# Kernel optimization log

Hardware: AMD Instinct MI355X
Metric: run time of the kernel (lower is better)

The kernel has to match this reference:

```python
import jax, jax.numpy as jnp
import numpy as np

B, LQ, C = 2, 12240, 256
NH, NL, NP = 8, 4, 4          # heads, levels, points
D = C // NH                   # head dim = 32
SHAPES = np.array([[96, 96], [48, 48], [24, 24], [12, 12]], dtype=np.int32)
LEN_IN = int((SHAPES[:, 0] * SHAPES[:, 1]).sum())  # 12240


def setup_inputs() -> dict:
    key = jax.random.key(0)
    ks = jax.random.split(key, 10)
    start = np.concatenate([[0], np.cumsum(SHAPES[:, 0] * SHAPES[:, 1])[:-1]]).astype(np.int32)
    return {
        "query": jax.random.normal(ks[0], (B, LQ, C), jnp.float32),
        "reference_points": jax.random.uniform(ks[1], (B, LQ, NL, 2), jnp.float32),
        "input_flatten": jax.random.normal(ks[2], (B, LEN_IN, C), jnp.float32),
        "input_spatial_shapes": jnp.asarray(SHAPES),
        "input_level_start_index": jnp.asarray(start),
        # params (sampling_offsets weight kept small so samples land near the reference point)
        "W_off": jax.random.normal(ks[3], (C, NH * NL * NP * 2), jnp.float32) * 0.01,
        "b_off": jax.random.normal(ks[4], (NH * NL * NP * 2,), jnp.float32) * 0.1,
        "W_attn": jax.random.normal(ks[5], (C, NH * NL * NP), jnp.float32) * 0.02,
        "b_attn": jnp.zeros((NH * NL * NP,), jnp.float32),
        "W_val": jax.random.normal(ks[6], (C, C), jnp.float32) * (1.0 / np.sqrt(C)),
        "b_val": jnp.zeros((C,), jnp.float32),
        "W_out": jax.random.normal(ks[7], (C, C), jnp.float32) * (1.0 / np.sqrt(C)),
        "b_out": jnp.zeros((C,), jnp.float32),
    }


def _bilinear_sample(v, loc):
    """grid_sample(align_corners=False, padding=zeros) equivalent.
    v:   (B, Hl, Wl, NH, D) level feature map per head
    loc: (B, Lq, NH, NP, 2) normalized sampling locations in [0,1]
    ->   (B, Lq, NH, NP, D)
    """
    _, Hl, Wl, _, _ = v.shape
    x = loc[..., 0] * Wl - 0.5
    y = loc[..., 1] * Hl - 0.5
    x0 = jnp.floor(x); y0 = jnp.floor(y)
    lx = x - x0;       ly = y - y0
    x0i = x0.astype(jnp.int32); y0i = y0.astype(jnp.int32)
    bi = jnp.arange(v.shape[0])[:, None, None, None]
    hi = jnp.arange(NH)[None, None, :, None]

    def gather(yi, xi):
        valid = (yi >= 0) & (yi < Hl) & (xi >= 0) & (xi < Wl)
        yc = jnp.clip(yi, 0, Hl - 1)
        xc = jnp.clip(xi, 0, Wl - 1)
        g = v[bi, yc, xc, hi]                       # (B,Lq,NH,NP,D)
        return g * valid[..., None].astype(v.dtype)

    w00 = (1 - lx) * (1 - ly); w01 = lx * (1 - ly)
    w10 = (1 - lx) * ly;       w11 = lx * ly
    return (gather(y0i, x0i) * w00[..., None] + gather(y0i, x0i + 1) * w01[..., None]
            + gather(y0i + 1, x0i) * w10[..., None] + gather(y0i + 1, x0i + 1) * w11[..., None])


def reference(query, reference_points, input_flatten, input_spatial_shapes,
              input_level_start_index, W_off, b_off, W_attn, b_attn,
              W_val, b_val, W_out, b_out):
    shapes = np.asarray(input_spatial_shapes)          # static level geometry
    starts = np.asarray(input_level_start_index)

    value = (input_flatten @ W_val + b_val).reshape(B, LEN_IN, NH, D)
    offsets = (query @ W_off + b_off).reshape(B, LQ, NH, NL, NP, 2)
    attn = (query @ W_attn + b_attn).reshape(B, LQ, NH, NL * NP)
    attn = jax.nn.softmax(attn, axis=-1).reshape(B, LQ, NH, NL, NP)

    # normalizer is (W_l, H_l) per level
    normalizer = jnp.stack([input_spatial_shapes[:, 1], input_spatial_shapes[:, 0]], -1).astype(query.dtype)
    loc = (reference_points[:, :, None, :, None, :]
           + offsets / normalizer[None, None, None, :, None, :])  # (B,Lq,NH,NL,NP,2)

    out = jnp.zeros((B, LQ, NH, D), query.dtype)
    for l in range(NL):
        Hl, Wl = int(shapes[l, 0]), int(shapes[l, 1])
        s = int(starts[l])
        v_l = value[:, s:s + Hl * Wl].reshape(B, Hl, Wl, NH, D)
        sampled = _bilinear_sample(v_l, loc[:, :, :, l])            # (B,Lq,NH,NP,D)
        out = out + jnp.einsum("bqhpd,bqhp->bqhd", sampled, attn[:, :, :, l])
    out = out.reshape(B, LQ, C)
    return out @ W_out + b_out
```

## Files before the change

kernel.cpp:

```cpp
#include <hip/hip_runtime.h>
#include <math.h>

#define B_    2
#define LQ_   12240
#define C_    256
#define NH_   8
#define NL_   4
#define NP_   4
#define LEN_IN_ 12240
#define MROWS (B_*LQ_)
#define MF_   (MROWS/16)
#define KF_   8
#define APLANE ((size_t)MROWS * C_)
#define NBLK  383

typedef __attribute__((ext_vector_type(8))) short short8v;
typedef __attribute__((ext_vector_type(4))) float f32x4;
typedef __attribute__((ext_vector_type(2))) float f32x2;
typedef __attribute__((ext_vector_type(2))) uint  u32x2;

__device__ __forceinline__ ushort f2bf_hi(float f) {
    uint u = __builtin_bit_cast(uint, f);
    uint r = (u + 0x7fffu + ((u >> 16) & 1u)) >> 16;
    return (ushort)r;
}
__device__ __forceinline__ float bf2f(ushort h) {
    uint u = ((uint)h) << 16;
    return __builtin_bit_cast(float, u);
}

#define U4_VAL  0
#define U4_OFF  8192
#define U4_ATT  16384
#define U4_UHI  20480
#define U4_ULO  28672
#define PACKB_TOTAL 294912

__global__ __launch_bounds__(256) void pack_w_kernel(
    const float* __restrict__ Wv, const float* __restrict__ Wo,
    const float* __restrict__ Wa, const float* __restrict__ Wu,
    ushort* __restrict__ packB)
{
    int gid = blockIdx.x * 256 + threadIdx.x;
    if (gid >= 28672) return;
    const float* W; ushort* hi; ushort* lo = nullptr; int N, rel;
    if (gid < 8192)       { W = Wv; hi = packB;          N = 256; rel = gid; }
    else if (gid < 16384) { W = Wo; hi = packB + 65536;  N = 256; rel = gid - 8192; }
    else if (gid < 20480) { W = Wa; hi = packB + 131072; N = 128; rel = gid - 16384; }
    else { W = Wu; hi = packB + 163840; lo = packB + 229376; N = 256; rel = gid - 20480; }

    const int lane = rel & 63;
    const int kf   = (rel >> 6) & 7;
    const int nf   = rel >> 9;
    const int row0 = kf * 32 + (lane >> 4) * 8;
    const int col  = nf * 16 + (lane & 15);

    union { ushort u16[8]; uint4 u4; } ch, cl;
#pragma unroll
    for (int j = 0; j < 8; ++j) {
        float x = W[(size_t)(row0 + j) * N + col];
        ushort h = f2bf_hi(x);
        ch.u16[j] = h;
        cl.u16[j] = f2bf_hi(x - bf2f(h));
    }
    *reinterpret_cast<uint4*>(hi + (size_t)rel * 8) = ch.u4;
    if (lo) *reinterpret_cast<uint4*>(lo + (size_t)rel * 8) = cl.u4;
}

__global__ __launch_bounds__(512) void gemm_vq_kernel(
    const float* __restrict__ inflat, const float* __restrict__ query,
    const ushort* __restrict__ packB,
    const float* __restrict__ b_val, const float* __restrict__ b_off,
    const float* __restrict__ b_attn,
    ushort* __restrict__ valbf, float* __restrict__ offsb, float* __restrict__ attnb)
{
    const int t = threadIdx.x, lane = t & 63, wid = t >> 6;
    const int rowBase = blockIdx.x * 64;
    const bool isVal = (blockIdx.y == 0);
    const float* __restrict__ A = isVal ? inflat : query;

    __shared__ ushort Als[2048 * 8];

#pragma unroll
    for (int i = 0; i < 4; ++i) {
        int frag = i * 512 + t;
        int fl = frag & 63, kf = (frag >> 6) & 7, mf = frag >> 9;
        int row = min(rowBase + mf * 16 + (fl & 15), MROWS - 1);
        int k0 = kf * 32 + (fl >> 4) * 8;
        const float4* s = reinterpret_cast<const float4*>(A + (size_t)row * 256 + k0);
        float4 v0 = s[0], v1 = s[1];
        float vv[8] = { v0.x, v0.y, v0.z, v0.w, v1.x, v1.y, v1.z, v1.w };
        union { ushort u16[8]; uint4 u4; } hh;
#pragma unroll
        for (int j = 0; j < 8; ++j) hh.u16[j] = f2bf_hi(vv[j]);
        *reinterpret_cast<uint4*>(&Als[(size_t)frag * 8]) = hh.u4;
    }
    __syncthreads();

    const uint4* A4 = reinterpret_cast<const uint4*>(Als);
    const int colLane = lane & 15, rquad = lane >> 4;
    const int wnf = wid * 2;

    if (isVal) {
        const uint4* B4 = reinterpret_cast<const uint4*>(packB) + U4_VAL;
        f32x4 acc[4][2];
#pragma unroll
        for (int mi = 0; mi < 4; ++mi)
#pragma unroll
            for (int f = 0; f < 2; ++f) acc[mi][f] = (f32x4)0.0f;

#pragma unroll
        for (int kf = 0; kf < KF_; ++kf) {
            uint4 bh[2], ah[4];
#pragma unroll
            for (int f = 0; f < 2; ++f) bh[f] = B4[((wnf + f) * KF_ + kf) * 64 + lane];
#pragma unroll
            for (int mi = 0; mi < 4; ++mi) ah[mi] = A4[(mi * KF_ + kf) * 64 + lane];
#pragma unroll
            for (int mi = 0; mi < 4; ++mi) {
                short8v a = __builtin_bit_cast(short8v, ah[mi]);
#pragma unroll
                for (int f = 0; f < 2; ++f)
                    acc[mi][f] = __builtin_amdgcn_mfma_f32_16x16x32_bf16(
                        a, __builtin_bit_cast(short8v, bh[f]), acc[mi][f], 0, 0, 0);
            }
        }
#pragma unroll
        for (int f = 0; f < 2; ++f) {
            int col = (wnf + f) * 16 + colLane;
            float bv = b_val[col];
#pragma unroll
            for (int mi = 0; mi < 4; ++mi)
#pragma unroll
                for (int e = 0; e < 4; ++e) {
                    int row = rowBase + mi * 16 + rquad * 4 + e;
                    if (row < MROWS) valbf[(size_t)row * 256 + col] = f2bf_hi(acc[mi][f][e] + bv);
                }
        }
    } else {
        const uint4* BO = reinterpret_cast<const uint4*>(packB) + U4_OFF;
        const uint4* BA = reinterpret_cast<const uint4*>(packB) + U4_ATT;
        f32x4 acc[4][3];
#pragma unroll
        for (int mi = 0; mi < 4; ++mi)
#pragma unroll
            for (int f = 0; f < 3; ++f) acc[mi][f] = (f32x4)0.0f;

#pragma unroll
        for (int kf = 0; kf < KF_; ++kf) {
            uint4 bh[3], ah[4];
#pragma unroll
            for (int f = 0; f < 2; ++f) bh[f] = BO[((wnf + f) * KF_ + kf) * 64 + lane];
            bh[2] = BA[(wid * KF_ + kf) * 64 + lane];
#pragma unroll
            for (int mi = 0; mi < 4; ++mi) ah[mi] = A4[(mi * KF_ + kf) * 64 + lane];
#pragma unroll
            for (int mi = 0; mi < 4; ++mi) {
                short8v a = __builtin_bit_cast(short8v, ah[mi]);
#pragma unroll
                for (int f = 0; f < 3; ++f)
                    acc[mi][f] = __builtin_amdgcn_mfma_f32_16x16x32_bf16(
                        a, __builtin_bit_cast(short8v, bh[f]), acc[mi][f], 0, 0, 0);
            }
        }
#pragma unroll
        for (int f = 0; f < 2; ++f) {
            int col = (wnf + f) * 16 + colLane;
            float bv = b_off[col];
#pragma unroll
            for (int mi = 0; mi < 4; ++mi)
#pragma unroll
                for (int e = 0; e < 4; ++e) {
                    int row = rowBase + mi * 16 + rquad * 4 + e;
                    if (row < MROWS) offsb[(size_t)row * 256 + col] = acc[mi][f][e] + bv;
                }
        }
        {
            int col = wid * 16 + colLane;
            float bv = b_attn[col];
#pragma unroll
            for (int mi = 0; mi < 4; ++mi)
#pragma unroll
                for (int e = 0; e < 4; ++e) {
                    float v = acc[mi][2][e] + bv;
                    float mx = v;
#pragma unroll
                    for (int m = 8; m >= 1; m >>= 1) mx = fmaxf(mx, __shfl_xor(mx, m, 16));
                    float ex = __expf(v - mx);
                    float s = ex;
#pragma unroll
                    for (int m = 8; m >= 1; m >>= 1) s += __shfl_xor(s, m, 16);
                    int row = rowBase + mi * 16 + rquad * 4 + e;
                    if (row < MROWS) attnb[(size_t)row * 128 + col] = ex / s;
                }
        }
    }
}

__global__ __launch_bounds__(512) void gemm_out_kernel(
    const ushort* __restrict__ midH, const ushort* __restrict__ packB,
    const float* __restrict__ bias, float* __restrict__ Cg)
{
    const int t = threadIdx.x, lane = t & 63, wid = t >> 6;
    const int rowBase = blockIdx.x * 64;

    __shared__ ushort Ahs[2048 * 8];

    const uint4* H4 = reinterpret_cast<const uint4*>(midH);
#pragma unroll
    for (int i = 0; i < 4; ++i) {
        int frag = i * 512 + t;
        int fl = frag & 63, kf = (frag >> 6) & 7, mf = frag >> 9;
        int row = min(rowBase + mf * 16 + (fl & 15), MROWS - 1);
        int kq = kf * 4 + (fl >> 4);
        *reinterpret_cast<uint4*>(&Ahs[(size_t)frag * 8]) = H4[(size_t)row * 32 + kq];
    }
    __syncthreads();

    const uint4* BH4 = reinterpret_cast<const uint4*>(packB) + U4_UHI;
    const uint4* BL4 = reinterpret_cast<const uint4*>(packB) + U4_ULO;
    const uint4* A4 = reinterpret_cast<const uint4*>(Ahs);
    const int wnf = wid * 2;

    f32x4 acc[4][2];
#pragma unroll
    for (int mi = 0; mi < 4; ++mi)
#pragma unroll
        for (int f = 0; f < 2; ++f) acc[mi][f] = (f32x4)0.0f;

#pragma unroll
    for (int kf = 0; kf < KF_; ++kf) {
        uint4 bh[2], bl[2], ah[4];
#pragma unroll
        for (int f = 0; f < 2; ++f) {
            bh[f] = BH4[((wnf + f) * KF_ + kf) * 64 + lane];
            bl[f] = BL4[((wnf + f) * KF_ + kf) * 64 + lane];
        }
#pragma unroll
        for (int mi = 0; mi < 4; ++mi) ah[mi] = A4[(mi * KF_ + kf) * 64 + lane];
#pragma unroll
        for (int mi = 0; mi < 4; ++mi) {
            short8v a = __builtin_bit_cast(short8v, ah[mi]);
#pragma unroll
            for (int f = 0; f < 2; ++f) {
                acc[mi][f] = __builtin_amdgcn_mfma_f32_16x16x32_bf16(
                    a, __builtin_bit_cast(short8v, bh[f]), acc[mi][f], 0, 0, 0);
                acc[mi][f] = __builtin_amdgcn_mfma_f32_16x16x32_bf16(
                    a, __builtin_bit_cast(short8v, bl[f]), acc[mi][f], 0, 0, 0);
            }
        }
    }

    const int colLane = lane & 15, rquad = lane >> 4;
#pragma unroll
    for (int f = 0; f < 2; ++f) {
        int col = (wnf + f) * 16 + colLane;
        float bv = bias[col];
#pragma unroll
        for (int mi = 0; mi < 4; ++mi)
#pragma unroll
            for (int e = 0; e < 4; ++e) {
                int row = rowBase + mi * 16 + rquad * 4 + e;
                if (row < MROWS) Cg[(size_t)row * 256 + col] = acc[mi][f][e] + bv;
            }
    }
}

__global__ __launch_bounds__(128) void sampler_kernel(
    const ushort* __restrict__ value,
    const float* __restrict__ offs,
    const float* __restrict__ attnw,
    const float* __restrict__ refp,
    ushort* __restrict__ midH)
{
    const int t  = threadIdx.x;
    const int qi = t >> 6;
    const int t6 = t & 63;
    const int q  = blockIdx.x * 2 + qi;

    __shared__ float s_ref[2][8];
    __shared__ int   s_addr[2][576];
    __shared__ float s_w[2][576];

    if (t < 16) s_ref[t >> 3][t & 7] = refp[(size_t)(blockIdx.x * 2 + (t >> 3)) * 8 + (t & 7)];
    __syncthreads();

#pragma unroll
    for (int batch = 0; batch < 2; ++batch) {
        const int p  = t6 + batch * 64;
        const int h  = p >> 4;
        const int lp = p & 15;
        const int l  = lp >> 2;

        const float aw = attnw[(size_t)q * 128 + p];
        const float2 o = reinterpret_cast<const float2*>(offs)[(size_t)q * 128 + p];
        const float rx = s_ref[qi][l * 2 + 0];
        const float ry = s_ref[qi][l * 2 + 1];

        const int   Wl = 96 >> l;
        const int   st = 12288 - (12288 >> (2 * l));
        const float fW = (float)Wl;

        const float x = fmaf(rx, fW, o.x) - 0.5f;
        const float y = fmaf(ry, fW, o.y) - 0.5f;
        const float x0f = floorf(x), y0f = floorf(y);
        const float fx = x - x0f, fy = y - y0f;
        const int x0 = (int)x0f, y0 = (int)y0f;
        const int x1 = x0 + 1,   y1 = y0 + 1;

        const float vx0 = (x0 >= 0 && x0 < Wl) ? 1.f : 0.f;
        const float vx1 = (x1 >= 0 && x1 < Wl) ? 1.f : 0.f;
        const float vy0 = (y0 >= 0 && y0 < Wl) ? 1.f : 0.f;
        const float vy1 = (y1 >= 0 && y1 < Wl) ? 1.f : 0.f;

        const int xc0 = min(max(x0, 0), Wl - 1);
        const int xc1 = min(max(x1, 0), Wl - 1);
        const int yc0 = min(max(y0, 0), Wl - 1);
        const int yc1 = min(max(y1, 0), Wl - 1);

        const int row0 = st + yc0 * Wl;
        const int row1 = st + yc1 * Wl;
        const int hb   = h << 5;

        const int sidx = (lp * 9 + h) * 4;
        int4 a;
        a.x = ((row0 + xc0) << 8) + hb;
        a.y = ((row0 + xc1) << 8) + hb;
        a.z = ((row1 + xc0) << 8) + hb;
        a.w = ((row1 + xc1) << 8) + hb;
        *reinterpret_cast<int4*>(&s_addr[qi][sidx]) = a;

        float4 w;
        w.x = aw * (1.f - fx) * (1.f - fy) * vx0 * vy0;
        w.y = aw * fx * (1.f - fy) * vx1 * vy0;
        w.z = aw * (1.f - fx) * fy * vx0 * vy1;
        w.w = aw * fx * fy * vx1 * vy1;
        *reinterpret_cast<float4*>(&s_w[qi][sidx]) = w;
    }
    __syncthreads();

    const int c2 = t6 >> 5;
    const int h  = (t6 >> 2) & 7;
    const int l2 = t6 & 3;
    const int d8 = l2 * 8;
    const ushort* __restrict__ vb = value + (q >= LQ_ ? (size_t)LEN_IN_ * 256 : 0) + d8;

    f32x2 aLo = (f32x2)0.f, aHi = (f32x2)0.f, bLo = (f32x2)0.f, bHi = (f32x2)0.f;

#pragma unroll
    for (int pt = 0; pt < 16; ++pt) {
        const int base = (pt * 9 + h) * 4 + c2 * 2;
        const int2   a = *reinterpret_cast<const int2*>(&s_addr[qi][base]);
        const float2 w = *reinterpret_cast<const float2*>(&s_w[qi][base]);
        uint4 v0 = *reinterpret_cast<const uint4*>(vb + a.x);
        uint4 v1 = *reinterpret_cast<const uint4*>(vb + a.y);
        f32x2 w0; w0.x = w.x; w0.y = w.x;
        f32x2 w1; w1.x = w.y; w1.y = w.y;

        u32x2 h01; h01.x = v0.x; h01.y = v0.y;
        u32x2 h23; h23.x = v0.z; h23.y = v0.w;
        u32x2 l01 = h01 << 16, l23 = h23 << 16;
        aHi = __builtin_elementwise_fma(__builtin_bit_cast(f32x2, h01), w0, aHi);
        aLo = __builtin_elementwise_fma(__builtin_bit_cast(f32x2, l01), w0, aLo);
        bHi = __builtin_elementwise_fma(__builtin_bit_cast(f32x2, h23), w0, bHi);
        bLo = __builtin_elementwise_fma(__builtin_bit_cast(f32x2, l23), w0, bLo);

        u32x2 g01; g01.x = v1.x; g01.y = v1.y;
        u32x2 g23; g23.x = v1.z; g23.y = v1.w;
        u32x2 m01 = g01 << 16, m23 = g23 << 16;
        aHi = __builtin_elementwise_fma(__builtin_bit_cast(f32x2, g01), w1, aHi);
        aLo = __builtin_elementwise_fma(__builtin_bit_cast(f32x2, m01), w1, aLo);
        bHi = __builtin_elementwise_fma(__builtin_bit_cast(f32x2, g23), w1, bHi);
        bLo = __builtin_elementwise_fma(__builtin_bit_cast(f32x2, m23), w1, bLo);
    }

    float r[8] = { aLo.x, aHi.x, aLo.y, aHi.y, bLo.x, bHi.x, bLo.y, bHi.y };
#pragma unroll
    for (int j = 0; j < 8; ++j) r[j] += __shfl_xor(r[j], 32);

    if (c2 == 0) {
        union { ushort u16[8]; uint4 u4; } hh;
#pragma unroll
        for (int j = 0; j < 8; ++j) hh.u16[j] = f2bf_hi(r[j]);
        *reinterpret_cast<uint4*>(midH + (size_t)q * 256 + (h << 5) + d8) = hh.u4;
    }
}

extern "C" void kernel_launch(void* const* d_in, const int* in_sizes, int n_in,
                              void* d_out, int out_size, void* d_ws, size_t ws_size,
                              hipStream_t stream)
{
    const float* query  = (const float*)d_in[0];
    const float* refp   = (const float*)d_in[1];
    const float* inflat = (const float*)d_in[2];
    const float* W_off  = (const float*)d_in[5];
    const float* b_off  = (const float*)d_in[6];
    const float* W_attn = (const float*)d_in[7];
    const float* b_attn = (const float*)d_in[8];
    const float* W_val  = (const float*)d_in[9];
    const float* b_val  = (const float*)d_in[10];
    const float* W_out  = (const float*)d_in[11];
    const float* b_out  = (const float*)d_in[12];
    float* out = (float*)d_out;

    ushort* midH  = (ushort*)d_ws;
    ushort* valbf = midH + APLANE;
    ushort* packB = valbf + APLANE;
    float*  offsb = (float*)(packB + PACKB_TOTAL);
    float*  attnb = offsb + APLANE;

    hipLaunchKernelGGL(pack_w_kernel, dim3(112), dim3(256), 0, stream,
                       W_val, W_off, W_attn, W_out, packB);
    hipLaunchKernelGGL(gemm_vq_kernel, dim3(NBLK, 2), dim3(512), 0, stream,
                       inflat, query, packB, b_val, b_off, b_attn,
                       valbf, offsb, attnb);
    hipLaunchKernelGGL(sampler_kernel, dim3(MROWS / 2), dim3(128), 0, stream,
                       valbf, offsb, attnb, refp, midH);
    hipLaunchKernelGGL(gemm_out_kernel, dim3(NBLK), dim3(512), 0, stream,
                       midH, packB, b_out, out);
}
```

Baseline: 89.20 us.

## Make GEMM kernels persistent with double-buffered LDS prefetch of next tile

Both the value/query projection GEMM and the output GEMM now launch a fixed grid of 128 blocks that loop over 64-row tiles. Each iteration issues the global loads for the next tile into registers before the MFMA work on the current tile, then writes them into a second LDS buffer. The aim is to overlap global-load latency with compute. In exchange, LDS doubles to 64 KB per block, register pressure rises, and the grid shrinks from 383 blocks, which leaves fewer blocks than the MI355X's CUs and can cause load imbalance (3 tiles for some blocks, 2 for others).

```diff
diff --git a/kernel.cpp b/kernel.cpp
--- a/kernel.cpp
+++ b/kernel.cpp
@@ -13,6 +13,7 @@
 #define KF_   8
 #define APLANE ((size_t)MROWS * C_)
 #define NBLK  383
+#define GRIDX 128
 
 typedef __attribute__((ext_vector_type(8))) short short8v;
 typedef __attribute__((ext_vector_type(4))) float f32x4;
@@ -75,125 +76,167 @@
     ushort* __restrict__ valbf, float* __restrict__ offsb, float* __restrict__ attnb)
 {
     const int t = threadIdx.x, lane = t & 63, wid = t >> 6;
-    const int rowBase = blockIdx.x * 64;
     const bool isVal = (blockIdx.y == 0);
     const float* __restrict__ A = isVal ? inflat : query;
 
-    __shared__ ushort Als[2048 * 8];
-
+    __shared__ ushort Als[2][2048 * 8];
+
+    int sfrag[4], srow[4], sk0[4];
 #pragma unroll
     for (int i = 0; i < 4; ++i) {
         int frag = i * 512 + t;
-        int fl = frag & 63, kf = (frag >> 6) & 7, mf = frag >> 9;
-        int row = min(rowBase + mf * 16 + (fl & 15), MROWS - 1);
-        int k0 = kf * 32 + (fl >> 4) * 8;
-        const float4* s = reinterpret_cast<const float4*>(A + (size_t)row * 256 + k0);
-        float4 v0 = s[0], v1 = s[1];
-        float vv[8] = { v0.x, v0.y, v0.z, v0.w, v1.x, v1.y, v1.z, v1.w };
-        union { ushort u16[8]; uint4 u4; } hh;
-#pragma unroll
-        for (int j = 0; j < 8; ++j) hh.u16[j] = f2bf_hi(vv[j]);
-        *reinterpret_cast<uint4*>(&Als[(size_t)frag * 8]) = hh.u4;
-    }
-    __syncthreads();
-
-    const uint4* A4 = reinterpret_cast<const uint4*>(Als);
+        sfrag[i] = frag;
+        int fl = frag & 63;
+        srow[i] = (frag >> 9) * 16 + (fl & 15);
+        sk0[i]  = ((frag >> 6) & 7) * 32 + (fl >> 4) * 8;
+    }
+
     const int colLane = lane & 15, rquad = lane >> 4;
     const int wnf = wid * 2;
 
-    if (isVal) {
-        const uint4* B4 = reinterpret_cast<const uint4*>(packB) + U4_VAL;
-        f32x4 acc[4][2];
-#pragma unroll
-        for (int mi = 0; mi < 4; ++mi)
-#pragma unroll
-            for (int f = 0; f < 2; ++f) acc[mi][f] = (f32x4)0.0f;
-
-#pragma unroll
-        for (int kf = 0; kf < KF_; ++kf) {
-            uint4 bh[2], ah[4];
-#pragma unroll
-            for (int f = 0; f < 2; ++f) bh[f] = B4[((wnf + f) * KF_ + kf) * 64 + lane];
-#pragma unroll
-            for (int mi = 0; mi < 4; ++mi) ah[mi] = A4[(mi * KF_ + kf) * 64 + lane];
-#pragma unroll
-            for (int mi = 0; mi < 4; ++mi) {
-                short8v a = __builtin_bit_cast(short8v, ah[mi]);
-#pragma unroll
-                for (int f = 0; f < 2; ++f)
-                    acc[mi][f] = __builtin_amdgcn_mfma_f32_16x16x32_bf16(
-                        a, __builtin_bit_cast(short8v, bh[f]), acc[mi][f], 0, 0, 0);
-            }
-        }
-#pragma unroll
-        for (int f = 0; f < 2; ++f) {
-            int col = (wnf + f) * 16 + colLane;
-            float bv = b_val[col];
+    float4 ld[4][2];
+#pragma unroll
+    for (int i = 0; i < 4; ++i) {
+        int row = min(blockIdx.x * 64 + srow[i], MROWS - 1);
+        const float4* s = reinterpret_cast<const float4*>(A + (size_t)row * 256 + sk0[i]);
+        ld[i][0] = s[0]; ld[i][1] = s[1];
+    }
+#pragma unroll
+    for (int i = 0; i < 4; ++i) {
+        float vv[8] = { ld[i][0].x, ld[i][0].y, ld[i][0].z, ld[i][0].w,
+                        ld[i][1].x, ld[i][1].y, ld[i][1].z, ld[i][1].w };
+        union { ushort u16[8]; uint4 u4; } hh;
+#pragma unroll
+        for (int j = 0; j < 8; ++j) hh.u16[j] = f2bf_hi(vv[j]);
+        *reinterpret_cast<uint4*>(&Als[0][(size_t)sfrag[i] * 8]) = hh.u4;
+    }
+    __syncthreads();
+
+    int buf = 0;
+    for (int tile = blockIdx.x; tile < NBLK; tile += GRIDX) {
+        const int rowBase = tile * 64;
+        const bool hasNext = (tile + GRIDX) < NBLK;
+
+        if (hasNext) {
+            int nrb = (tile + GRIDX) * 64;
+#pragma unroll
+            for (int i = 0; i < 4; ++i) {
+                int row = min(nrb + srow[i], MROWS - 1);
+                const float4* s = reinterpret_cast<const float4*>(A + (size_t)row * 256 + sk0[i]);
+                ld[i][0] = s[0]; ld[i][1] = s[1];
+            }
+        }
+
+        const uint4* A4 = reinterpret_cast<const uint4*>(Als[buf]);
+
+        if (isVal) {
+            const uint4* B4 = reinterpret_cast<const uint4*>(packB) + U4_VAL;
+            f32x4 acc[4][2];
 #pragma unroll
             for (int mi = 0; mi < 4; ++mi)
 #pragma unroll
-                for (int e = 0; e < 4; ++e) {
-                    int row = rowBase + mi * 16 + rquad * 4 + e;
-                    if (row < MROWS) valbf[(size_t)row * 256 + col] = f2bf_hi(acc[mi][f][e] + bv);
+                for (int f = 0; f < 2; ++f) acc[mi][f] = (f32x4)0.0f;
+
+#pragma unroll
+            for (int kf = 0; kf < KF_; ++kf) {
+                uint4 bh[2], ah[4];
+#pragma unroll
+                for (int f = 0; f < 2; ++f) bh[f] = B4[((wnf + f) * KF_ + kf) * 64 + lane];
+#pragma unroll
+                for (int mi = 0; mi < 4; ++mi) ah[mi] = A4[(mi * KF_ + kf) * 64 + lane];
+#pragma unroll
+                for (int mi = 0; mi < 4; ++mi) {
+                    short8v a = __builtin_bit_cast(short8v, ah[mi]);
+#pragma unroll
+                    for (int f = 0; f < 2; ++f)
+                        acc[mi][f] = __builtin_amdgcn_mfma_f32_16x16x32_bf16(
+                            a, __builtin_bit_cast(short8v, bh[f]), acc[mi][f], 0, 0, 0);
                 }
-        }
-    } else {
-        const uint4* BO = reinterpret_cast<const uint4*>(packB) + U4_OFF;
-        const uint4* BA = reinterpret_cast<const uint4*>(packB) + U4_ATT;
-        f32x4 acc[4][3];
-#pragma unroll
-        for (int mi = 0; mi < 4; ++mi)
-#pragma unroll
-            for (int f = 0; f < 3; ++f) acc[mi][f] = (f32x4)0.0f;
-
-#pragma unroll
-        for (int kf = 0; kf < KF_; ++kf) {
-            uint4 bh[3], ah[4];
-#pragma unroll
-            for (int f = 0; f < 2; ++f) bh[f] = BO[((wnf + f) * KF_ + kf) * 64 + lane];
-            bh[2] = BA[(wid * KF_ + kf) * 64 + lane];
-#pragma unroll
-            for (int mi = 0; mi < 4; ++mi) ah[mi] = A4[(mi * KF_ + kf) * 64 + lane];
-#pragma unroll
-            for (int mi = 0; mi < 4; ++mi) {
-                short8v a = __builtin_bit_cast(short8v, ah[mi]);
-#pragma unroll
-                for (int f = 0; f < 3; ++f)
-                    acc[mi][f] = __builtin_amdgcn_mfma_f32_16x16x32_bf16(
-                        a, __builtin_bit_cast(short8v, bh[f]), acc[mi][f], 0, 0, 0);
-            }
-        }
-#pragma unroll
-        for (int f = 0; f < 2; ++f) {
-            int col = (wnf + f) * 16 + colLane;
-            float bv = b_off[col];
+            }
+#pragma unroll
+            for (int f = 0; f < 2; ++f) {
+                int col = (wnf + f) * 16 + colLane;
+                float bv = b_val[col];
+#pragma unroll
+                for (int mi = 0; mi < 4; ++mi)
+#pragma unroll
+                    for (int e = 0; e < 4; ++e) {
+                        int row = rowBase + mi * 16 + rquad * 4 + e;
+                        if (row < MROWS) valbf[(size_t)row * 256 + col] = f2bf_hi(acc[mi][f][e] + bv);
+                    }
+            }
+        } else {
+            const uint4* BO = reinterpret_cast<const uint4*>(packB) + U4_OFF;
+            const uint4* BA = reinterpret_cast<const uint4*>(packB) + U4_ATT;
+            f32x4 acc[4][3];
 #pragma unroll
             for (int mi = 0; mi < 4; ++mi)
 #pragma unroll
-                for (int e = 0; e < 4; ++e) {
-                    int row = rowBase + mi * 16 + rquad * 4 + e;
-                    if (row < MROWS) offsb[(size_t)row * 256 + col] = acc[mi][f][e] + bv;
+                for (int f = 0; f < 3; ++f) acc[mi][f] = (f32x4)0.0f;
+
+#pragma unroll
+            for (int kf = 0; kf < KF_; ++kf) {
+                uint4 bh[3], ah[4];
+#pragma unroll
+                for (int f = 0; f < 2; ++f) bh[f] = BO[((wnf + f) * KF_ + kf) * 64 + lane];
+                bh[2] = BA[(wid * KF_ + kf) * 64 + lane];
+#pragma unroll
+                for (int mi = 0; mi < 4; ++mi) ah[mi] = A4[(mi * KF_ + kf) * 64 + lane];
+#pragma unroll
+                for (int mi = 0; mi < 4; ++mi) {
+                    short8v a = __builtin_bit_cast(short8v, ah[mi]);
+#pragma unroll
+                    for (int f = 0; f < 3; ++f)
+                        acc[mi][f] = __builtin_amdgcn_mfma_f32_16x16x32_bf16(
+                            a, __builtin_bit_cast(short8v, bh[f]), acc[mi][f], 0, 0, 0);
                 }
-        }
-        {
-            int col = wid * 16 + colLane;
-            float bv = b_attn[col];
-#pragma unroll
-            for (int mi = 0; mi < 4; ++mi)
-#pragma unroll
-                for (int e = 0; e < 4; ++e) {
-                    float v = acc[mi][2][e] + bv;
-                    float mx = v;
-#pragma unroll
-                    for (int m = 8; m >= 1; m >>= 1) mx = fmaxf(mx, __shfl_xor(mx, m, 16));
-                    float ex = __expf(v - mx);
-                    float s = ex;
-#pragma unroll
-                    for (int m = 8; m >= 1; m >>= 1) s += __shfl_xor(s, m, 16);
-                    int row = rowBase + mi * 16 + rquad * 4 + e;
-                    if (row < MROWS) attnb[(size_t)row * 128 + col] = ex / s;
-                }
-        }
+            }
+#pragma unroll
+            for (int f = 0; f < 2; ++f) {
+                int col = (wnf + f) * 16 + colLane;
+                float bv = b_off[col];
+#pragma unroll
+                for (int mi = 0; mi < 4; ++mi)
+#pragma unroll
+                    for (int e = 0; e < 4; ++e) {
+                        int row = rowBase + mi * 16 + rquad * 4 + e;
+                        if (row < MROWS) offsb[(size_t)row * 256 + col] = acc[mi][f][e] + bv;
+                    }
+            }
+            {
+                int col = wid * 16 + colLane;
+                float bv = b_attn[col];
+#pragma unroll
+                for (int mi = 0; mi < 4; ++mi)
+#pragma unroll
+                    for (int e = 0; e < 4; ++e) {
+                        float v = acc[mi][2][e] + bv;
+                        float mx = v;
+#pragma unroll
+                        for (int m = 8; m >= 1; m >>= 1) mx = fmaxf(mx, __shfl_xor(mx, m, 16));
+                        float ex = __expf(v - mx);
+                        float s = ex;
+#pragma unroll
+                        for (int m = 8; m >= 1; m >>= 1) s += __shfl_xor(s, m, 16);
+                        int row = rowBase + mi * 16 + rquad * 4 + e;
+                        if (row < MROWS) attnb[(size_t)row * 128 + col] = ex / s;
+                    }
+            }
+        }
+
+        if (hasNext) {
+#pragma unroll
+            for (int i = 0; i < 4; ++i) {
+                float vv[8] = { ld[i][0].x, ld[i][0].y, ld[i][0].z, ld[i][0].w,
+                                ld[i][1].x, ld[i][1].y, ld[i][1].z, ld[i][1].w };
+                union { ushort u16[8]; uint4 u4; } hh;
+#pragma unroll
+                for (int j = 0; j < 8; ++j) hh.u16[j] = f2bf_hi(vv[j]);
+                *reinterpret_cast<uint4*>(&Als[buf ^ 1][(size_t)sfrag[i] * 8]) = hh.u4;
+            }
+        }
+        __syncthreads();
+        buf ^= 1;
     }
 }
 
@@ -202,67 +245,102 @@
     const float* __restrict__ bias, float* __restrict__ Cg)
 {
     const int t = threadIdx.x, lane = t & 63, wid = t >> 6;
-    const int rowBase = blockIdx.x * 64;
-
-    __shared__ ushort Ahs[2048 * 8];
-
-    const uint4* H4 = reinterpret_cast<const uint4*>(midH);
+
+    __shared__ ushort Ahs[2][2048 * 8];
+
+    int sfrag[4], srow[4], skq[4];
 #pragma unroll
     for (int i = 0; i < 4; ++i) {
         int frag = i * 512 + t;
-        int fl = frag & 63, kf = (frag >> 6) & 7, mf = frag >> 9;
-        int row = min(rowBase + mf * 16 + (fl & 15), MROWS - 1);
-        int kq = kf * 4 + (fl >> 4);
-        *reinterpret_cast<uint4*>(&Ahs[(size_t)frag * 8]) = H4[(size_t)row * 32 + kq];
-    }
+        sfrag[i] = frag;
+        int fl = frag & 63;
+        srow[i] = (frag >> 9) * 16 + (fl & 15);
+        skq[i]  = ((frag >> 6) & 7) * 4 + (fl >> 4);
+    }
+
+    const uint4* H4 = reinterpret_cast<const uint4*>(midH);
+    const int colLane = lane & 15, rquad = lane >> 4;
+    const int wnf = wid * 2;
+
+    uint4 ld[4];
+#pragma unroll
+    for (int i = 0; i < 4; ++i) {
+        int row = min(blockIdx.x * 64 + srow[i], MROWS - 1);
+        ld[i] = H4[(size_t)row * 32 + skq[i]];
+    }
+#pragma unroll
+    for (int i = 0; i < 4; ++i)
+        *reinterpret_cast<uint4*>(&Ahs[0][(size_t)sfrag[i] * 8]) = ld[i];
     __syncthreads();
 
     const uint4* BH4 = reinterpret_cast<const uint4*>(packB) + U4_UHI;
     const uint4* BL4 = reinterpret_cast<const uint4*>(packB) + U4_ULO;
-    const uint4* A4 = reinterpret_cast<const uint4*>(Ahs);
-    const int wnf = wid * 2;
-
-    f32x4 acc[4][2];
-#pragma unroll
-    for (int mi = 0; mi < 4; ++mi)
-#pragma unroll
-        for (int f = 0; f < 2; ++f) acc[mi][f] = (f32x4)0.0f;
-
-#pragma unroll
-    for (int kf = 0; kf < KF_; ++kf) {
-        uint4 bh[2], bl[2], ah[4];
+
+    int buf = 0;
+    for (int tile = blockIdx.x; tile < NBLK; tile += GRIDX) {
+        const int rowBase = tile * 64;
+        const bool hasNext = (tile + GRIDX) < NBLK;
+
+        if (hasNext) {
+            int nrb = (tile + GRIDX) * 64;
+#pragma unroll
+            for (int i = 0; i < 4; ++i) {
+                int row = min(nrb + srow[i], MROWS - 1);
+                ld[i] = H4[(size_t)row * 32 + skq[i]];
+            }
+        }
+
+        const uint4* A4 = reinterpret_cast<const uint4*>(Ahs[buf]);
+
+        f32x4 acc[4][2];
+#pragma unroll
+        for (int mi = 0; mi < 4; ++mi)
+#pragma unroll
+            for (int f = 0; f < 2; ++f) acc[mi][f] = (f32x4)0.0f;
+
+#pragma unroll
+        for (int kf = 0; kf < KF_; ++kf) {
+            uint4 bh[2], bl[2], ah[4];
+#pragma unroll
+            for (int f = 0; f < 2; ++f) {
+                bh[f] = BH4[((wnf + f) * KF_ + kf) * 64 + lane];
+                bl[f] = BL4[((wnf + f) * KF_ + kf) * 64 + lane];
+            }
+#pragma unroll
+            for (int mi = 0; mi < 4; ++mi) ah[mi] = A4[(mi * KF_ + kf) * 64 + lane];
+#pragma unroll
+            for (int mi = 0; mi < 4; ++mi) {
+                short8v a = __builtin_bit_cast(short8v, ah[mi]);
+#pragma unroll
+                for (int f = 0; f < 2; ++f) {
+                    acc[mi][f] = __builtin_amdgcn_mfma_f32_16x16x32_bf16(
+                        a, __builtin_bit_cast(short8v, bh[f]), acc[mi][f], 0, 0, 0);
+                    acc[mi][f] = __builtin_amdgcn_mfma_f32_16x16x32_bf16(
+                        a, __builtin_bit_cast(short8v, bl[f]), acc[mi][f], 0, 0, 0);
+                }
+            }
+        }
+
 #pragma unroll
         for (int f = 0; f < 2; ++f) {
-            bh[f] = BH4[((wnf + f) * KF_ + kf) * 64 + lane];
-            bl[f] = BL4[((wnf + f) * KF_ + kf) * 64 + lane];
-        }
-#pragma unroll
-        for (int mi = 0; mi < 4; ++mi) ah[mi] = A4[(mi * KF_ + kf) * 64 + lane];
-#pragma unroll
-        for (int mi = 0; mi < 4; ++mi) {
-            short8v a = __builtin_bit_cast(short8v, ah[mi]);
-#pragma unroll
-            for (int f = 0; f < 2; ++f) {
-                acc[mi][f] = __builtin_amdgcn_mfma_f32_16x16x32_bf16(
-                    a, __builtin_bit_cast(short8v, bh[f]), acc[mi][f], 0, 0, 0);
-                acc[mi][f] = __builtin_amdgcn_mfma_f32_16x16x32_bf16(
-                    a, __builtin_bit_cast(short8v, bl[f]), acc[mi][f], 0, 0, 0);
-            }
-        }
-    }
-
-    const int colLane = lane & 15, rquad = lane >> 4;
-#pragma unroll
-    for (int f = 0; f < 2; ++f) {
-        int col = (wnf + f) * 16 + colLane;
-        float bv = bias[col];
-#pragma unroll
-        for (int mi = 0; mi < 4; ++mi)
-#pragma unroll
-            for (int e = 0; e < 4; ++e) {
-                int row = rowBase + mi * 16 + rquad * 4 + e;
-                if (row < MROWS) Cg[(size_t)row * 256 + col] = acc[mi][f][e] + bv;
-            }
+            int col = (wnf + f) * 16 + colLane;
+            float bv = bias[col];
+#pragma unroll
+            for (int mi = 0; mi < 4; ++mi)
+#pragma unroll
+                for (int e = 0; e < 4; ++e) {
+                    int row = rowBase + mi * 16 + rquad * 4 + e;
+                    if (row < MROWS) Cg[(size_t)row * 256 + col] = acc[mi][f][e] + bv;
+                }
+        }
+
+        if (hasNext) {
+#pragma unroll
+            for (int i = 0; i < 4; ++i)
+                *reinterpret_cast<uint4*>(&Ahs[buf ^ 1][(size_t)sfrag[i] * 8]) = ld[i];
+        }
+        __syncthreads();
+        buf ^= 1;
     }
 }
 
@@ -411,11 +489,11 @@
 
     hipLaunchKernelGGL(pack_w_kernel, dim3(112), dim3(256), 0, stream,
                        W_val, W_off, W_attn, W_out, packB);
-    hipLaunchKernelGGL(gemm_vq_kernel, dim3(NBLK, 2), dim3(512), 0, stream,
+    hipLaunchKernelGGL(gemm_vq_kernel, dim3(GRIDX, 2), dim3(512), 0, stream,
                        inflat, query, packB, b_val, b_off, b_attn,
                        valbf, offsb, attnb);
     hipLaunchKernelGGL(sampler_kernel, dim3(MROWS / 2), dim3(128), 0, stream,
                        valbf, offsb, attnb, refp, midH);
-    hipLaunchKernelGGL(gemm_out_kernel, dim3(NBLK), dim3(512), 0, stream,
+    hipLaunchKernelGGL(gemm_out_kernel, dim3(GRIDX), dim3(512), 0, stream,
                        midH, packB, b_out, out);
 }
```

Measured after the change: 106.1 us. 18.9% more time.

## Stage GEMM epilogues through LDS for coalesced stores; store offsets/attn as bf16

Applied to the files above, without the earlier changes.

All GEMM epilogues now write results into a padded shared-memory tile and then store full rows with 16-byte vector writes, replacing scattered 2- or 4-byte stores. The sampling offsets and attention weights are also stored as bf16 instead of fp32, halving that intermediate traffic, and the sampler widens them back to float. This adds extra barriers and LDS traffic in the epilogue and reduces the precision of the sampling offsets, which can shift sample locations.

```diff
diff --git a/kernel.cpp b/kernel.cpp
--- a/kernel.cpp
+++ b/kernel.cpp
@@ -36,6 +36,9 @@
 #define U4_ULO  28672
 #define PACKB_TOTAL 294912
 
+#define ESTRIDE 272
+#define FSTRIDE 268
+
 __global__ __launch_bounds__(256) void pack_w_kernel(
     const float* __restrict__ Wv, const float* __restrict__ Wo,
     const float* __restrict__ Wa, const float* __restrict__ Wu,
@@ -72,14 +75,14 @@
     const ushort* __restrict__ packB,
     const float* __restrict__ b_val, const float* __restrict__ b_off,
     const float* __restrict__ b_attn,
-    ushort* __restrict__ valbf, float* __restrict__ offsb, float* __restrict__ attnb)
+    ushort* __restrict__ valbf, ushort* __restrict__ offsb, ushort* __restrict__ attnb)
 {
     const int t = threadIdx.x, lane = t & 63, wid = t >> 6;
     const int rowBase = blockIdx.x * 64;
     const bool isVal = (blockIdx.y == 0);
     const float* __restrict__ A = isVal ? inflat : query;
 
-    __shared__ ushort Als[2048 * 8];
+    __shared__ ushort Sh[64 * ESTRIDE];
 
 #pragma unroll
     for (int i = 0; i < 4; ++i) {
@@ -93,11 +96,11 @@
         union { ushort u16[8]; uint4 u4; } hh;
 #pragma unroll
         for (int j = 0; j < 8; ++j) hh.u16[j] = f2bf_hi(vv[j]);
-        *reinterpret_cast<uint4*>(&Als[(size_t)frag * 8]) = hh.u4;
+        *reinterpret_cast<uint4*>(&Sh[(size_t)frag * 8]) = hh.u4;
     }
     __syncthreads();
 
-    const uint4* A4 = reinterpret_cast<const uint4*>(Als);
+    const uint4* A4 = reinterpret_cast<const uint4*>(Sh);
     const int colLane = lane & 15, rquad = lane >> 4;
     const int wnf = wid * 2;
 
@@ -125,6 +128,7 @@
                         a, __builtin_bit_cast(short8v, bh[f]), acc[mi][f], 0, 0, 0);
             }
         }
+        __syncthreads();
 #pragma unroll
         for (int f = 0; f < 2; ++f) {
             int col = (wnf + f) * 16 + colLane;
@@ -132,10 +136,17 @@
 #pragma unroll
             for (int mi = 0; mi < 4; ++mi)
 #pragma unroll
-                for (int e = 0; e < 4; ++e) {
-                    int row = rowBase + mi * 16 + rquad * 4 + e;
-                    if (row < MROWS) valbf[(size_t)row * 256 + col] = f2bf_hi(acc[mi][f][e] + bv);
-                }
+                for (int e = 0; e < 4; ++e)
+                    Sh[(mi * 16 + rquad * 4 + e) * ESTRIDE + col] = f2bf_hi(acc[mi][f][e] + bv);
+        }
+        __syncthreads();
+#pragma unroll
+        for (int i = 0; i < 4; ++i) {
+            int idx = i * 512 + t, row = idx >> 5, c8 = idx & 31;
+            int grow = rowBase + row;
+            if (grow < MROWS)
+                *reinterpret_cast<uint4*>(valbf + (size_t)grow * 256 + c8 * 8) =
+                    *reinterpret_cast<const uint4*>(&Sh[row * ESTRIDE + c8 * 8]);
         }
     } else {
         const uint4* BO = reinterpret_cast<const uint4*>(packB) + U4_OFF;
@@ -163,6 +174,7 @@
                         a, __builtin_bit_cast(short8v, bh[f]), acc[mi][f], 0, 0, 0);
             }
         }
+        __syncthreads();
 #pragma unroll
         for (int f = 0; f < 2; ++f) {
             int col = (wnf + f) * 16 + colLane;
@@ -170,11 +182,19 @@
 #pragma unroll
             for (int mi = 0; mi < 4; ++mi)
 #pragma unroll
-                for (int e = 0; e < 4; ++e) {
-                    int row = rowBase + mi * 16 + rquad * 4 + e;
-                    if (row < MROWS) offsb[(size_t)row * 256 + col] = acc[mi][f][e] + bv;
-                }
-        }
+                for (int e = 0; e < 4; ++e)
+                    Sh[(mi * 16 + rquad * 4 + e) * ESTRIDE + col] = f2bf_hi(acc[mi][f][e] + bv);
+        }
+        __syncthreads();
+#pragma unroll
+        for (int i = 0; i < 4; ++i) {
+            int idx = i * 512 + t, row = idx >> 5, c8 = idx & 31;
+            int grow = rowBase + row;
+            if (grow < MROWS)
+                *reinterpret_cast<uint4*>(offsb + (size_t)grow * 256 + c8 * 8) =
+                    *reinterpret_cast<const uint4*>(&Sh[row * ESTRIDE + c8 * 8]);
+        }
+        __syncthreads();
         {
             int col = wid * 16 + colLane;
             float bv = b_attn[col];
@@ -190,9 +210,17 @@
                     float s = ex;
 #pragma unroll
                     for (int m = 8; m >= 1; m >>= 1) s += __shfl_xor(s, m, 16);
-                    int row = rowBase + mi * 16 + rquad * 4 + e;
-                    if (row < MROWS) attnb[(size_t)row * 128 + col] = ex / s;
+                    Sh[(mi * 16 + rquad * 4 + e) * ESTRIDE + col] = f2bf_hi(ex / s);
                 }
+        }
+        __syncthreads();
+#pragma unroll
+        for (int i = 0; i < 2; ++i) {
+            int idx = i * 512 + t, row = idx >> 4, c8 = idx & 15;
+            int grow = rowBase + row;
+            if (grow < MROWS)
+                *reinterpret_cast<uint4*>(attnb + (size_t)grow * 128 + c8 * 8) =
+                    *reinterpret_cast<const uint4*>(&Sh[row * ESTRIDE + c8 * 8]);
         }
     }
 }
@@ -204,7 +232,7 @@
     const int t = threadIdx.x, lane = t & 63, wid = t >> 6;
     const int rowBase = blockIdx.x * 64;
 
-    __shared__ ushort Ahs[2048 * 8];
+    __shared__ ushort Sh[64 * ESTRIDE];
 
     const uint4* H4 = reinterpret_cast<const uint4*>(midH);
 #pragma unroll
@@ -213,13 +241,13 @@
         int fl = frag & 63, kf = (frag >> 6) & 7, mf = frag >> 9;
         int row = min(rowBase + mf * 16 + (fl & 15), MROWS - 1);
         int kq = kf * 4 + (fl >> 4);
-        *reinterpret_cast<uint4*>(&Ahs[(size_t)frag * 8]) = H4[(size_t)row * 32 + kq];
+        *reinterpret_cast<uint4*>(&Sh[(size_t)frag * 8]) = H4[(size_t)row * 32 + kq];
     }
     __syncthreads();
 
     const uint4* BH4 = reinterpret_cast<const uint4*>(packB) + U4_UHI;
     const uint4* BL4 = reinterpret_cast<const uint4*>(packB) + U4_ULO;
-    const uint4* A4 = reinterpret_cast<const uint4*>(Ahs);
+    const uint4* A4 = reinterpret_cast<const uint4*>(Sh);
     const int wnf = wid * 2;
 
     f32x4 acc[4][2];
@@ -252,24 +280,38 @@
     }
 
     const int colLane = lane & 15, rquad = lane >> 4;
-#pragma unroll
-    for (int f = 0; f < 2; ++f) {
-        int col = (wnf + f) * 16 + colLane;
-        float bv = bias[col];
-#pragma unroll
-        for (int mi = 0; mi < 4; ++mi)
-#pragma unroll
-            for (int e = 0; e < 4; ++e) {
-                int row = rowBase + mi * 16 + rquad * 4 + e;
-                if (row < MROWS) Cg[(size_t)row * 256 + col] = acc[mi][f][e] + bv;
+    float* ShF = reinterpret_cast<float*>(Sh);
+#pragma unroll
+    for (int phase = 0; phase < 2; ++phase) {
+        __syncthreads();
+#pragma unroll
+        for (int f = 0; f < 2; ++f) {
+            int col = (wnf + f) * 16 + colLane;
+            float bv = bias[col];
+#pragma unroll
+            for (int mi2 = 0; mi2 < 2; ++mi2) {
+                int mi = phase * 2 + mi2;
+#pragma unroll
+                for (int e = 0; e < 4; ++e)
+                    ShF[(mi2 * 16 + rquad * 4 + e) * FSTRIDE + col] = acc[mi][f][e] + bv;
             }
+        }
+        __syncthreads();
+#pragma unroll
+        for (int i = 0; i < 4; ++i) {
+            int idx = i * 512 + t, row = idx >> 6, c4 = idx & 63;
+            int grow = rowBase + phase * 32 + row;
+            if (grow < MROWS)
+                *reinterpret_cast<float4*>(Cg + (size_t)grow * 256 + c4 * 4) =
+                    *reinterpret_cast<const float4*>(&ShF[row * FSTRIDE + c4 * 4]);
+        }
     }
 }
 
 __global__ __launch_bounds__(128) void sampler_kernel(
     const ushort* __restrict__ value,
-    const float* __restrict__ offs,
-    const float* __restrict__ attnw,
+    const ushort* __restrict__ offs,
+    const ushort* __restrict__ attnw,
     const float* __restrict__ refp,
     ushort* __restrict__ midH)
 {
@@ -292,8 +334,10 @@
         const int lp = p & 15;
         const int l  = lp >> 2;
 
-        const float aw = attnw[(size_t)q * 128 + p];
-        const float2 o = reinterpret_cast<const float2*>(offs)[(size_t)q * 128 + p];
+        const float aw = bf2f(attnw[(size_t)q * 128 + p]);
+        const uint o2 = reinterpret_cast<const uint*>(offs)[(size_t)q * 128 + p];
+        const float ox = bf2f((ushort)(o2 & 0xffffu));
+        const float oy = bf2f((ushort)(o2 >> 16));
         const float rx = s_ref[qi][l * 2 + 0];
         const float ry = s_ref[qi][l * 2 + 1];
 
@@ -301,8 +345,8 @@
         const int   st = 12288 - (12288 >> (2 * l));
         const float fW = (float)Wl;
 
-        const float x = fmaf(rx, fW, o.x) - 0.5f;
-        const float y = fmaf(ry, fW, o.y) - 0.5f;
+        const float x = fmaf(rx, fW, ox) - 0.5f;
+        const float y = fmaf(ry, fW, oy) - 0.5f;
         const float x0f = floorf(x), y0f = floorf(y);
         const float fx = x - x0f, fy = y - y0f;
         const int x0 = (int)x0f, y0 = (int)y0f;
@@ -406,8 +450,8 @@
     ushort* midH  = (ushort*)d_ws;
     ushort* valbf = midH + APLANE;
     ushort* packB = valbf + APLANE;
-    float*  offsb = (float*)(packB + PACKB_TOTAL);
-    float*  attnb = offsb + APLANE;
+    ushort* offsb = packB + PACKB_TOTAL;
+    ushort* attnb = offsb + APLANE;
 
     hipLaunchKernelGGL(pack_w_kernel, dim3(112), dim3(256), 0, stream,
                        W_val, W_off, W_attn, W_out, packB);
```

Result: faster. 79.87 us (-10.5%).
